# Kernel optimization log

Measured on AMD Instinct MI355X. Metric: run time of the kernel, lower is better.

The kernel has to match this reference:

```python
import jax, jax.numpy as jnp
import numpy as np

# Model constants (from init_kwargs)
NF, NC, E, B = 100000, 4000, 500000, 256
D_FACT, D_COMP = 1536, 27
HIDDEN, HEADS, CPH = 128, 4, 32  # out_per_head = hidden // heads
NUM_LAYERS = 2
TIME_DIM = 8
T_SCALE = 30.0
EDGE_DIM = 2 + TIME_DIM  # [sentiment, decay, time2vec]
ATTN_SCALE = 1.0  # 1 / attn_temperature
NEG_SLOPE = 0.2


def time_edge_features(ea, lam):
    # ea: [E, 2] = [sentiment, decay]; second column in [0,1] -> decay branch
    s = jnp.clip(ea[:, 0:1], -1.0, 1.0)
    decay = jnp.clip(ea[:, 1:2], 0.0, 1.0)
    lam = jnp.maximum(lam, 1e-6)
    delta_t = -jnp.log(jnp.maximum(decay, 1e-6)) / lam
    t = jnp.log1p(jnp.maximum(delta_t, 0.0)) / T_SCALE  # [E,1]
    freqs = jnp.arange(1, TIME_DIM, dtype=ea.dtype)      # [TIME_DIM-1]
    sins = jnp.sin(t * freqs)                            # [E,TIME_DIM-1]
    return jnp.concatenate([s, decay, sins, t], axis=-1)  # [E, EDGE_DIM]


def seg_softmax(logits, seg, n):
    # logits: [E,H]; softmax over edges sharing the same destination node
    m = jax.ops.segment_max(logits, seg, num_segments=n)
    z = jnp.exp(logits - m[seg])
    den = jax.ops.segment_sum(z, seg, num_segments=n)
    return z / (den[seg] + 1e-16)


def seg_mean(x, seg, n):
    s = jax.ops.segment_sum(x, seg, num_segments=n)
    cnt = jax.ops.segment_sum(jnp.ones((x.shape[0],), x.dtype), seg, num_segments=n)
    return s / jnp.maximum(cnt, 1.0)[:, None]


def layernorm(x, g, b, eps=1e-5):
    mu = jnp.mean(x, axis=-1, keepdims=True)
    var = jnp.var(x, axis=-1, keepdims=True)
    return (x - mu) * jax.lax.rsqrt(var + eps) * g + b


def setup_inputs() -> dict:
    key = jax.random.key(0)
    ks = jax.random.split(key, 32)

    x_fact = jax.random.normal(ks[0], (NF, D_FACT), jnp.float32)
    x_company = jax.random.normal(ks[1], (NC, D_COMP), jnp.float32)
    u = jax.random.uniform(ks[2], (E, 2), jnp.float32)
    edge_attr = jnp.concatenate([u[:, 0:1] * 2.0 - 1.0, u[:, 1:2]], axis=1)
    edge_index = jnp.stack([
        jax.random.randint(ks[3], (E,), 0, NF),
        jax.random.randint(ks[4], (E,), 0, NC),
    ]).astype(jnp.int32)
    batch_fact = jnp.sort(jax.random.randint(ks[5], (NF,), 0, B)).astype(jnp.int32)
    batch_company = jnp.sort(jax.random.randint(ks[6], (NC,), 0, B)).astype(jnp.int32)

    def p(k, shape):
        return jax.random.normal(k, shape, jnp.float32) * 0.05

    inp = dict(
        x_fact=x_fact, x_company=x_company, edge_attr=edge_attr,
        edge_index=edge_index, batch_fact=batch_fact, batch_company=batch_company,
        lambda_decay=jnp.array(0.01, jnp.float32),
        Wf=p(ks[7], (D_FACT, HIDDEN)), bf=jnp.zeros((HIDDEN,), jnp.float32),
        Wc=p(ks[8], (D_COMP, HIDDEN)), bc=jnp.zeros((HIDDEN,), jnp.float32),
        Wl=p(ks[9], (NUM_LAYERS, HIDDEN, HIDDEN)), bl=jnp.zeros((NUM_LAYERS, HIDDEN), jnp.float32),
        Wr=p(ks[10], (NUM_LAYERS, HIDDEN, HIDDEN)), br=jnp.zeros((NUM_LAYERS, HIDDEN), jnp.float32),
        We=p(ks[11], (NUM_LAYERS, EDGE_DIM, HIDDEN)), be=jnp.zeros((NUM_LAYERS, HIDDEN), jnp.float32),
        att=p(ks[12], (NUM_LAYERS, HEADS, CPH)),
        bias_out=jnp.zeros((NUM_LAYERS, HIDDEN), jnp.float32),
        ln_g=jnp.ones((NUM_LAYERS, HIDDEN), jnp.float32), ln_b=jnp.zeros((NUM_LAYERS, HIDDEN), jnp.float32),
        Wg=p(ks[13], (2 * HIDDEN, 1)), bg=jnp.zeros((1,), jnp.float32),
        W1=p(ks[14], (HIDDEN, HIDDEN)), b1=jnp.zeros((HIDDEN,), jnp.float32),
        W2=p(ks[15], (HIDDEN, 1)), b2=jnp.zeros((1,), jnp.float32),
    )
    return inp


def reference(x_fact, x_company, edge_attr, edge_index, batch_fact, batch_company,
              lambda_decay, Wf, bf, Wc, bc, Wl, bl, Wr, br, We, be, att, bias_out,
              ln_g, ln_b, Wg, bg, W1, b1, W2, b2):
    src, dst = edge_index[0], edge_index[1]
    ef = time_edge_features(edge_attr, lambda_decay)          # [E, EDGE_DIM]

    # per-node-type input encoders
    hf = jax.nn.relu(x_fact @ Wf + bf)                         # [NF, H]
    hc = jax.nn.relu(x_company @ Wc + bc)                      # [NC, H]
    n_c = x_company.shape[0]

    for l in range(NUM_LAYERS):
        # GATv2 (edge-conditioned, bipartite fact->company, share_weights=False)
        gl = (hf @ Wl[l] + bl[l]).reshape(-1, HEADS, CPH)      # src transform [NF,H,C]
        gr = (hc @ Wr[l] + br[l]).reshape(-1, HEADS, CPH)      # dst transform [NC,H,C]
        ge = (ef @ We[l] + be[l]).reshape(-1, HEADS, CPH)      # edge transform [E,H,C]
        e = jax.nn.leaky_relu(gl[src] + gr[dst] + ge, NEG_SLOPE)  # [E,H,C]
        logits = jnp.einsum('ehc,hc->eh', e, att[l]) * ATTN_SCALE  # [E,H]
        alpha = seg_softmax(logits, dst, n_c)                   # scatter-softmax over dst
        msg = alpha[..., None] * gl[src]                        # [E,H,C]
        out = jax.ops.segment_sum(msg, dst, num_segments=n_c).reshape(n_c, HIDDEN) + bias_out[l]
        hc = layernorm(hc + jax.nn.relu(out), ln_g[l], ln_b[l])  # residual + post-norm

    # gated readout over graphs in batch
    pf = seg_mean(hf, batch_fact, B)                            # [B,H]
    pc = seg_mean(hc, batch_company, B)                         # [B,H]
    g = jax.nn.sigmoid(jnp.concatenate([pf, pc], axis=-1) @ Wg + bg)  # [B,1]
    h = g * pf + (1.0 - g) * pc                                 # [B,H]
    logit = jax.nn.relu(h @ W1 + b1) @ W2 + b2                  # [B,1]
    return logit
```

## Files before the change

kernel.cpp:

```cpp
#include <hip/hip_runtime.h>
#include <hip/hip_bf16.h>
#include <math.h>

#define NFAC 100000
#define NCOMP 4000
#define NEDGE 500000
#define NB 256
#define DF 1536
#define DC 27
#define H 128
#define EDIM 10

typedef __attribute__((ext_vector_type(8))) short short8v;
typedef __attribute__((ext_vector_type(4))) float f32x4;

#define GLOAD_LDS16(g, l)                                                              \
  __builtin_amdgcn_global_load_lds((const __attribute__((address_space(1))) unsigned int*)(g), \
                                   (__attribute__((address_space(3))) unsigned int*)(l), 16, 0, 0)

__device__ __forceinline__ float group32_sum(float v) {
#pragma unroll
  for (int m = 16; m > 0; m >>= 1) v += __shfl_xor(v, m);
  return v;
}

__device__ __forceinline__ unsigned short bf16rn(float x) {
  unsigned int u = __float_as_uint(x);
  unsigned int r = (u + 0x7fffu + ((u >> 16) & 1u)) >> 16;
  return (unsigned short)r;
}
__device__ __forceinline__ float bf16tof(unsigned short h) {
  return __uint_as_float(((unsigned int)h) << 16);
}

__global__ void k_edge_feat(const float* __restrict__ ea, const float* __restrict__ lamp,
                            float* __restrict__ ef) {
  int e = blockIdx.x * blockDim.x + threadIdx.x;
  if (e >= NEDGE) return;
  float s   = fminf(fmaxf(ea[2 * e], -1.f), 1.f);
  float dec = fminf(fmaxf(ea[2 * e + 1], 0.f), 1.f);
  float lam = fmaxf(lamp[0], 1e-6f);
  float dt  = -logf(fmaxf(dec, 1e-6f)) / lam;
  float t   = log1pf(fmaxf(dt, 0.f)) * (1.f / 30.f);
  float* o = ef + (size_t)e * EDIM;
  o[0] = s;
  o[1] = dec;
#pragma unroll
  for (int k = 1; k < 8; k++) o[1 + k] = __sinf(t * (float)k);
  o[9] = t;
}

__global__ void k_hist(const int* __restrict__ dst, int* __restrict__ deg) {
  int e = blockIdx.x * blockDim.x + threadIdx.x;
  if (e < NEDGE) atomicAdd(&deg[dst[e]], 1);
}

__global__ __launch_bounds__(1024) void k_scan(const int* __restrict__ deg, int* __restrict__ off) {
  __shared__ int s[4096];
  int t = threadIdx.x;
  for (int i = t; i < 4096; i += 1024) s[i] = (i < NCOMP) ? deg[i] : 0;
  __syncthreads();
  for (int d = 1; d < 4096; d <<= 1) {
    int vals[4];
#pragma unroll
    for (int j = 0; j < 4; j++) {
      int i = t + j * 1024;
      vals[j] = (i >= d) ? s[i - d] : 0;
    }
    __syncthreads();
#pragma unroll
    for (int j = 0; j < 4; j++) {
      int i = t + j * 1024;
      s[i] += vals[j];
    }
    __syncthreads();
  }
  for (int i = t; i < 4096; i += 1024) off[i + 1] = s[i];
  if (t == 0) off[0] = 0;
}

__global__ void k_scatter(const int* __restrict__ dst, const int* __restrict__ off,
                          int* __restrict__ cur, int* __restrict__ eid) {
  int e = blockIdx.x * blockDim.x + threadIdx.x;
  if (e < NEDGE) {
    int d = dst[e];
    int p = atomicAdd(&cur[d], 1);
    eid[off[d] + p] = e;
  }
}

__global__ void k_conv_w(const float* __restrict__ W, unsigned short* __restrict__ Bh,
                         unsigned short* __restrict__ Bl, int K) {
  int i = blockIdx.x * blockDim.x + threadIdx.x;
  if (i >= K * H) return;
  int k = i >> 7, c = i & 127;
  float x = W[i];
  unsigned short h = bf16rn(x);
  unsigned short l = bf16rn(x - bf16tof(h));
  Bh[(size_t)c * K + k] = h;
  Bl[(size_t)c * K + k] = l;
}

__device__ __forceinline__ unsigned int packhi(unsigned int u1, unsigned int u0) {
  return __builtin_amdgcn_perm(u1, u0, 0x07060302u);
}

__global__ __launch_bounds__(256, 2) void k_gemm_mfma(const float* __restrict__ A,
                                                      const unsigned short* __restrict__ Bth,
                                                      const unsigned short* __restrict__ Btl,
                                                      const float* __restrict__ bias,
                                                      float* __restrict__ C, int M, int K,
                                                      int dorelu, float* __restrict__ Cpart) {
  __shared__ __align__(16) char smem[2][32768];
  int tid = threadIdx.x;
  int wave = tid >> 6, lane = tid & 63;
  int m0 = blockIdx.x * 128;
  int wm = (wave >> 1) * 64, wn = (wave & 1) * 64;
  int fr = lane & 15, fg = lane >> 4;
  int nsplit = gridDim.y;
  int Ks = K / nsplit;
  int kbeg = blockIdx.y * Ks;
  int nIter = Ks >> 5;

  f32x4 acc[4][4];
#pragma unroll
  for (int i = 0; i < 4; i++)
#pragma unroll
    for (int j = 0; j < 4; j++) acc[i][j] = (f32x4){0.f, 0.f, 0.f, 0.f};

  int a_row = (lane >> 3);
  int a_s = lane & 7;
  int b_col = (lane >> 2);
  int b_s = lane & 3;

  auto stage = [&](int buf, int k0) {
    char* base = smem[buf];
#pragma unroll
    for (int q = 0; q < 4; q++) {
      int j = wave + 4 * q;
      int row = j * 8 + a_row;
      int grow = m0 + row;
      if (grow >= M) grow = 0;
      const float* src = A + (size_t)grow * K + k0 + ((a_s ^ (row & 7)) << 2);
      GLOAD_LDS16(src, base + j * 1024);
    }
#pragma unroll
    for (int q = 0; q < 2; q++) {
      int j = wave + 4 * q;
      int col = j * 16 + b_col;
      int soff = k0 + ((b_s ^ (col & 3)) << 3);
      GLOAD_LDS16(Bth + (size_t)col * K + soff, base + 16384 + j * 1024);
      GLOAD_LDS16(Btl + (size_t)col * K + soff, base + 24576 + j * 1024);
    }
  };

  stage(0, kbeg);
  __syncthreads();

  for (int it = 0; it < nIter; ++it) {
    int cur = it & 1;
    if (it + 1 < nIter) stage(cur ^ 1, kbeg + ((it + 1) << 5));
    const char* cb = smem[cur];
    short8v ah[4], al[4];
#pragma unroll
    for (int mf = 0; mf < 4; mf++) {
      int r = wm + 16 * mf + fr;
      int s0 = (2 * fg) ^ (r & 7);
      int s1 = (2 * fg + 1) ^ (r & 7);
      float4 a0 = *(const float4*)(cb + r * 128 + s0 * 16);
      float4 a1 = *(const float4*)(cb + r * 128 + s1 * 16);
      float xs[8] = {a0.x, a0.y, a0.z, a0.w, a1.x, a1.y, a1.z, a1.w};
      unsigned int hu[8], lu[8];
#pragma unroll
      for (int j = 0; j < 8; j++) {
        unsigned int u = __float_as_uint(xs[j]);
        hu[j] = u & 0xffff0000u;
        lu[j] = __float_as_uint(xs[j] - __uint_as_float(hu[j]));
      }
      unsigned int hw[4], lw[4];
#pragma unroll
      for (int j = 0; j < 4; j++) {
        hw[j] = packhi(hu[2 * j + 1], hu[2 * j]);
        lw[j] = packhi(lu[2 * j + 1], lu[2 * j]);
      }
      ah[mf] = *(short8v*)hw;
      al[mf] = *(short8v*)lw;
    }
#pragma unroll
    for (int nf = 0; nf < 4; nf++) {
      int c = wn + 16 * nf + fr;
      int sb = fg ^ (c & 3);
      short8v bh = *(const short8v*)(cb + 16384 + c * 64 + sb * 16);
      short8v bl = *(const short8v*)(cb + 24576 + c * 64 + sb * 16);
#pragma unroll
      for (int mf = 0; mf < 4; mf++) {
        acc[mf][nf] = __builtin_amdgcn_mfma_f32_16x16x32_bf16(ah[mf], bh, acc[mf][nf], 0, 0, 0);
        acc[mf][nf] = __builtin_amdgcn_mfma_f32_16x16x32_bf16(ah[mf], bl, acc[mf][nf], 0, 0, 0);
        acc[mf][nf] = __builtin_amdgcn_mfma_f32_16x16x32_bf16(al[mf], bh, acc[mf][nf], 0, 0, 0);
      }
    }
    __syncthreads();
  }

  if (nsplit == 1) {
#pragma unroll
    for (int mf = 0; mf < 4; mf++) {
      int rbase = m0 + wm + 16 * mf + 4 * fg;
#pragma unroll
      for (int nf = 0; nf < 4; nf++) {
        int col = wn + 16 * nf + fr;
        float bv = bias[col];
#pragma unroll
        for (int j = 0; j < 4; j++) {
          int row = rbase + j;
          if (row < M) {
            float v = acc[mf][nf][j] + bv;
            if (dorelu) v = fmaxf(v, 0.f);
            C[(size_t)row * H + col] = v;
          }
        }
      }
    }
  } else {
    float* P = Cpart + (size_t)blockIdx.y * M * H;
#pragma unroll
    for (int mf = 0; mf < 4; mf++) {
      int rbase = m0 + wm + 16 * mf + 4 * fg;
#pragma unroll
      for (int nf = 0; nf < 4; nf++) {
        int col = wn + 16 * nf + fr;
#pragma unroll
        for (int j = 0; j < 4; j++) {
          int row = rbase + j;
          if (row < M) P[(size_t)row * H + col] = acc[mf][nf][j];
        }
      }
    }
  }
}

__global__ __launch_bounds__(256) void k_reduce2(const float* __restrict__ P0,
                                                 const float* __restrict__ P1,
                                                 const float* __restrict__ bias,
                                                 float* __restrict__ C, int total4) {
  int i = blockIdx.x * blockDim.x + threadIdx.x;
  if (i >= total4) return;
  float4 a = ((const float4*)P0)[i];
  float4 b = ((const float4*)P1)[i];
  float4 bv = ((const float4*)bias)[i & 31];
  float4 r;
  r.x = fmaxf(a.x + b.x + bv.x, 0.f);
  r.y = fmaxf(a.y + b.y + bv.y, 0.f);
  r.z = fmaxf(a.z + b.z + bv.z, 0.f);
  r.w = fmaxf(a.w + b.w + bv.w, 0.f);
  ((float4*)C)[i] = r;
}

__global__ void k_enc_comp(const float* __restrict__ X, const float* __restrict__ Wc,
                           const float* __restrict__ bc, float* __restrict__ hc) {
  int tid = threadIdx.x;
  int r = blockIdx.x * 2 + (tid >> 7);
  int j = tid & 127;
  if (r >= NCOMP) return;
  float acc = bc[j];
  const float* x = X + (size_t)r * DC;
#pragma unroll
  for (int k = 0; k < DC; k++) acc = fmaf(x[k], Wc[k * H + j], acc);
  hc[(size_t)r * H + j] = fmaxf(acc, 0.f);
}

__global__ __launch_bounds__(128) void k_node(
    const float* __restrict__ gl, const float* __restrict__ ef, const int* __restrict__ srcArr,
    const int* __restrict__ csr_off, const int* __restrict__ csr_eid,
    const float* __restrict__ Wr, const float* __restrict__ br, const float* __restrict__ We,
    const float* __restrict__ be, const float* __restrict__ att,
    const float* __restrict__ bias_out, const float* __restrict__ lng,
    const float* __restrict__ lnb, float* __restrict__ hc) {
  int v = blockIdx.x;
  int t = threadIdx.x;
  __shared__ float hcs[H];
  __shared__ float WeS[EDIM * H];
  __shared__ float red[2], redq[2];
  float x = hc[(size_t)v * H + t];
  hcs[t] = x;
#pragma unroll
  for (int i = 0; i < EDIM; i++) WeS[i * H + t] = We[i * H + t];
  __syncthreads();
  float grv = br[t];
  for (int k = 0; k < H; k++) grv = fmaf(hcs[k], Wr[k * H + t], grv);
  float attv = att[t];
  float bev = be[t];
  int e0 = csr_off[v], e1 = csr_off[v + 1];
  float m = -INFINITY, s = 0.f, acc = 0.f;
  for (int i = e0; i < e1; ++i) {
    int eid = csr_eid[i];
    int sid = srcArr[eid];
    float glv = gl[(size_t)sid * H + t];
    const float* efr = ef + (size_t)eid * EDIM;
    float ge = bev;
#pragma unroll
    for (int k = 0; k < EDIM; k++) ge = fmaf(efr[k], WeS[k * H + t], ge);
    float ev = glv + grv + ge;
    ev = ev > 0.f ? ev : 0.2f * ev;
    float logit = group32_sum(ev * attv);
    float mn = fmaxf(m, logit);
    float scale = __expf(m - mn);
    float z = __expf(logit - mn);
    s = s * scale + z;
    acc = acc * scale + z * glv;
    m = mn;
  }
  float outv = acc / (s + 1e-16f);
  outv += bias_out[t];
  outv = fmaxf(outv, 0.f);
  float y = x + outv;
  float sv = y, qv = y * y;
#pragma unroll
  for (int mm = 32; mm > 0; mm >>= 1) {
    sv += __shfl_xor(sv, mm);
    qv += __shfl_xor(qv, mm);
  }
  int wid = t >> 6, lane = t & 63;
  if (lane == 0) {
    red[wid] = sv;
    redq[wid] = qv;
  }
  __syncthreads();
  float mean = (red[0] + red[1]) * (1.f / H);
  float var = (redq[0] + redq[1]) * (1.f / H) - mean * mean;
  float r = rsqrtf(var + 1e-5f);
  hc[(size_t)v * H + t] = (y - mean) * r * lng[t] + lnb[t];
}

template <int CHUNK>
__global__ __launch_bounds__(128) void k_segmean(const float* __restrict__ X,
                                                 const int* __restrict__ seg, int n,
                                                 float* __restrict__ sum, int* __restrict__ cnt) {
  int t = threadIdx.x;
  int n0 = blockIdx.x * CHUNK;
  int n1 = min(n0 + CHUNK, n);
  float acc = 0.f;
  int c = 0;
  int curs = -1;
  for (int i = n0; i < n1; ++i) {
    int sg = seg[i];
    if (sg != curs) {
      if (curs >= 0) {
        atomicAdd(&sum[(size_t)curs * H + t], acc);
        if (t == 0) atomicAdd(&cnt[curs], c);
      }
      curs = sg;
      acc = 0.f;
      c = 0;
    }
    acc += X[(size_t)i * H + t];
    c++;
  }
  if (curs >= 0) {
    atomicAdd(&sum[(size_t)curs * H + t], acc);
    if (t == 0) atomicAdd(&cnt[curs], c);
  }
}

__global__ __launch_bounds__(128) void k_readout(const float* __restrict__ pf,
                                                 const float* __restrict__ pc,
                                                 const int* __restrict__ cf,
                                                 const int* __restrict__ cc,
                                                 const float* __restrict__ Wg,
                                                 const float* __restrict__ bg,
                                                 const float* __restrict__ W1,
                                                 const float* __restrict__ b1,
                                                 const float* __restrict__ W2,
                                                 const float* __restrict__ b2,
                                                 float* __restrict__ out) {
  int b = blockIdx.x, t = threadIdx.x;
  __shared__ float hs[H];
  __shared__ float red[2], red2[2];
  int wid = t >> 6, lane = t & 63;
  float nf = fmaxf((float)cf[b], 1.f);
  float nc = fmaxf((float)cc[b], 1.f);
  float pfv = pf[(size_t)b * H + t] / nf;
  float pcv = pc[(size_t)b * H + t] / nc;
  float gp = pfv * Wg[t] + pcv * Wg[H + t];
  float sv = gp;
#pragma unroll
  for (int mm = 32; mm > 0; mm >>= 1) sv += __shfl_xor(sv, mm);
  if (lane == 0) red[wid] = sv;
  __syncthreads();
  float g = 1.f / (1.f + expf(-(red[0] + red[1] + bg[0])));
  float h = g * pfv + (1.f - g) * pcv;
  hs[t] = h;
  __syncthreads();
  float a = b1[t];
  for (int k = 0; k < H; k++) a = fmaf(hs[k], W1[k * H + t], a);
  a = fmaxf(a, 0.f);
  float p = a * W2[t];
#pragma unroll
  for (int mm = 32; mm > 0; mm >>= 1) p += __shfl_xor(p, mm);
  if (lane == 0) red2[wid] = p;
  __syncthreads();
  if (t == 0) out[b] = red2[0] + red2[1] + b2[0];
}

extern "C" void kernel_launch(void* const* d_in, const int* in_sizes, int n_in, void* d_out,
                              int out_size, void* d_ws, size_t ws_size, hipStream_t stream) {
  const float* x_fact = (const float*)d_in[0];
  const float* x_comp = (const float*)d_in[1];
  const float* ea = (const float*)d_in[2];
  const int* eidx = (const int*)d_in[3];
  const int* batf = (const int*)d_in[4];
  const int* batc = (const int*)d_in[5];
  const float* lam = (const float*)d_in[6];
  const float* Wf = (const float*)d_in[7];
  const float* bf = (const float*)d_in[8];
  const float* Wc = (const float*)d_in[9];
  const float* bc = (const float*)d_in[10];
  const float* Wl = (const float*)d_in[11];
  const float* bl = (const float*)d_in[12];
  const float* Wr = (const float*)d_in[13];
  const float* br_ = (const float*)d_in[14];
  const float* We = (const float*)d_in[15];
  const float* be = (const float*)d_in[16];
  const float* att = (const float*)d_in[17];
  const float* b_out = (const float*)d_in[18];
  const float* lng = (const float*)d_in[19];
  const float* lnb = (const float*)d_in[20];
  const float* Wg = (const float*)d_in[21];
  const float* bg = (const float*)d_in[22];
  const float* W1 = (const float*)d_in[23];
  const float* b1 = (const float*)d_in[24];
  const float* W2 = (const float*)d_in[25];
  const float* b2 = (const float*)d_in[26];
  float* out = (float*)d_out;

  char* w = (char*)d_ws;
  auto carve = [&](size_t bytes) -> char* {
    char* p = w;
    w += (bytes + 255) & ~(size_t)255;
    return p;
  };
  float* HF = (float*)carve((size_t)NFAC * H * 4);
  float* GL = (float*)carve((size_t)NFAC * H * 4);
  float* CP1 = (float*)carve((size_t)NFAC * H * 4);
  float* HC = (float*)carve((size_t)NCOMP * H * 4);
  float* EF = (float*)carve((size_t)NEDGE * EDIM * 4);
  int* OFF = (int*)carve(4100 * 4);
  int* EID = (int*)carve((size_t)NEDGE * 4);
  unsigned short* WfH = (unsigned short*)carve((size_t)DF * H * 2);
  unsigned short* WfL = (unsigned short*)carve((size_t)DF * H * 2);
  unsigned short* WlH[2], *WlL[2];
  for (int l = 0; l < 2; l++) {
    WlH[l] = (unsigned short*)carve((size_t)H * H * 2);
    WlL[l] = (unsigned short*)carve((size_t)H * H * 2);
  }
  char* zbase = w;
  int* DEG = (int*)carve(4096 * 4);
  int* CUR = (int*)carve(4096 * 4);
  float* PF = (float*)carve((size_t)NB * H * 4);
  float* PC = (float*)carve((size_t)NB * H * 4);
  int* CF = (int*)carve(NB * 4);
  int* CC = (int*)carve(NB * 4);
  size_t zbytes = (size_t)(w - zbase);
  hipMemsetAsync(zbase, 0, zbytes, stream);

  const int* srcArr = eidx;
  const int* dstArr = eidx + NEDGE;

  k_edge_feat<<<(NEDGE + 255) / 256, 256, 0, stream>>>(ea, lam, EF);
  k_hist<<<(NEDGE + 255) / 256, 256, 0, stream>>>(dstArr, DEG);
  k_scan<<<1, 1024, 0, stream>>>(DEG, OFF);
  k_scatter<<<(NEDGE + 255) / 256, 256, 0, stream>>>(dstArr, OFF, CUR, EID);

  k_conv_w<<<(DF * H + 255) / 256, 256, 0, stream>>>(Wf, WfH, WfL, DF);
  for (int l = 0; l < 2; l++)
    k_conv_w<<<(H * H + 255) / 256, 256, 0, stream>>>(Wl + (size_t)l * H * H, WlH[l], WlL[l], H);

  {
    float* CPART = GL;
    dim3 grid((NFAC + 127) / 128, 2);
    k_gemm_mfma<<<grid, 256, 0, stream>>>(x_fact, WfH, WfL, bf, HF, NFAC, DF, 1, CPART);
    int total4 = NFAC * H / 4;
    k_reduce2<<<(total4 + 255) / 256, 256, 0, stream>>>(GL, CP1, bf, HF, total4);
  }
  k_enc_comp<<<NCOMP / 2, 256, 0, stream>>>(x_comp, Wc, bc, HC);

  for (int l = 0; l < 2; l++) {
    dim3 grid((NFAC + 127) / 128, 1);
    k_gemm_mfma<<<grid, 256, 0, stream>>>(HF, WlH[l], WlL[l], bl + l * H, GL, NFAC, H, 0,
                                          (float*)nullptr);
    k_node<<<NCOMP, 128, 0, stream>>>(GL, EF, srcArr, OFF, EID, Wr + (size_t)l * H * H,
                                      br_ + l * H, We + (size_t)l * EDIM * H, be + l * H,
                                      att + l * H, b_out + l * H, lng + l * H, lnb + l * H, HC);
  }

  k_segmean<128><<<(NFAC + 127) / 128, 128, 0, stream>>>(HF, batf, NFAC, PF, CF);
  k_segmean<64><<<(NCOMP + 63) / 64, 128, 0, stream>>>(HC, batc, NCOMP, PC, CC);
  k_readout<<<NB, 128, 0, stream>>>(PF, PC, CF, CC, Wg, bg, W1, b1, W2, b2, out);
}
```

Measured before the change: 765.3 us.

## Split per-node edge loop across four thread groups with online-softmax merge

The node attention kernel now runs 512 threads per company node, with four 128-thread groups each handling every fourth incoming edge. Each group keeps its own running max, sum and accumulator, and these are merged through shared memory with a log-sum-exp combine before the residual and layernorm. The next edge's index and source id are also prefetched inside the loop to hide the dependent load latency. This shortens the serial chain of about 125 edges per node and adds parallelism. The cost is that each group recomputes the 128x128 Wr projection, and there is extra shared memory and a block barrier.

Result: slower. 844.1 us (+10.3%).

```diff
diff --git a/kernel.cpp b/kernel.cpp
--- a/kernel.cpp
+++ b/kernel.cpp
@@ -269,7 +269,8 @@
   hc[(size_t)r * H + j] = fmaxf(acc, 0.f);
 }
 
-__global__ __launch_bounds__(128) void k_node(
+#define NG 4
+__global__ __launch_bounds__(512) void k_node(
     const float* __restrict__ gl, const float* __restrict__ ef, const int* __restrict__ srcArr,
     const int* __restrict__ csr_off, const int* __restrict__ csr_eid,
     const float* __restrict__ Wr, const float* __restrict__ br, const float* __restrict__ We,
@@ -277,29 +278,44 @@
     const float* __restrict__ bias_out, const float* __restrict__ lng,
     const float* __restrict__ lnb, float* __restrict__ hc) {
   int v = blockIdx.x;
-  int t = threadIdx.x;
+  int tid = threadIdx.x;
+  int g = tid >> 7;
+  int t = tid & 127;
   __shared__ float hcs[H];
   __shared__ float WeS[EDIM * H];
+  __shared__ float gmA[NG][H];
+  __shared__ float gsA[NG][H];
+  __shared__ float gaA[NG][H];
   __shared__ float red[2], redq[2];
-  float x = hc[(size_t)v * H + t];
-  hcs[t] = x;
-#pragma unroll
-  for (int i = 0; i < EDIM; i++) WeS[i * H + t] = We[i * H + t];
-  __syncthreads();
+  if (tid < H) hcs[tid] = hc[(size_t)v * H + tid];
+  for (int i = tid; i < EDIM * H; i += 512) WeS[i] = We[i];
+  __syncthreads();
+
   float grv = br[t];
   for (int k = 0; k < H; k++) grv = fmaf(hcs[k], Wr[k * H + t], grv);
   float attv = att[t];
   float bev = be[t];
+
   int e0 = csr_off[v], e1 = csr_off[v + 1];
   float m = -INFINITY, s = 0.f, acc = 0.f;
-  for (int i = e0; i < e1; ++i) {
-    int eid = csr_eid[i];
-    int sid = srcArr[eid];
+  int i = e0 + g;
+  int eid = 0, sid = 0;
+  if (i < e1) {
+    eid = csr_eid[i];
+    sid = srcArr[eid];
+  }
+  while (i < e1) {
     float glv = gl[(size_t)sid * H + t];
     const float* efr = ef + (size_t)eid * EDIM;
     float ge = bev;
 #pragma unroll
     for (int k = 0; k < EDIM; k++) ge = fmaf(efr[k], WeS[k * H + t], ge);
+    int ni = i + NG;
+    if (ni < e1) {
+      int ne = csr_eid[ni];
+      eid = ne;
+      sid = srcArr[ne];
+    }
     float ev = glv + grv + ge;
     ev = ev > 0.f ? ev : 0.2f * ev;
     float logit = group32_sum(ev * attv);
@@ -309,27 +325,48 @@
     s = s * scale + z;
     acc = acc * scale + z * glv;
     m = mn;
-  }
-  float outv = acc / (s + 1e-16f);
-  outv += bias_out[t];
-  outv = fmaxf(outv, 0.f);
-  float y = x + outv;
-  float sv = y, qv = y * y;
-#pragma unroll
-  for (int mm = 32; mm > 0; mm >>= 1) {
-    sv += __shfl_xor(sv, mm);
-    qv += __shfl_xor(qv, mm);
-  }
-  int wid = t >> 6, lane = t & 63;
-  if (lane == 0) {
-    red[wid] = sv;
-    redq[wid] = qv;
-  }
-  __syncthreads();
-  float mean = (red[0] + red[1]) * (1.f / H);
-  float var = (redq[0] + redq[1]) * (1.f / H) - mean * mean;
-  float r = rsqrtf(var + 1e-5f);
-  hc[(size_t)v * H + t] = (y - mean) * r * lng[t] + lnb[t];
+    i = ni;
+  }
+  gmA[g][t] = m;
+  gsA[g][t] = s;
+  gaA[g][t] = acc;
+  __syncthreads();
+
+  float y = 0.f;
+  if (tid < H) {
+    float mstar = gmA[0][t];
+#pragma unroll
+    for (int q = 1; q < NG; q++) mstar = fmaxf(mstar, gmA[q][t]);
+    float sstar = 0.f, astar = 0.f;
+#pragma unroll
+    for (int q = 0; q < NG; q++) {
+      float mg = gmA[q][t];
+      float w = (mg > -INFINITY) ? __expf(mg - mstar) : 0.f;
+      sstar += gsA[q][t] * w;
+      astar += gaA[q][t] * w;
+    }
+    float outv = astar / (sstar + 1e-16f);
+    outv += bias_out[t];
+    outv = fmaxf(outv, 0.f);
+    y = hcs[t] + outv;
+    float sv = y, qv = y * y;
+#pragma unroll
+    for (int mm = 32; mm > 0; mm >>= 1) {
+      sv += __shfl_xor(sv, mm);
+      qv += __shfl_xor(qv, mm);
+    }
+    if ((t & 63) == 0) {
+      red[t >> 6] = sv;
+      redq[t >> 6] = qv;
+    }
+  }
+  __syncthreads();
+  if (tid < H) {
+    float mean = (red[0] + red[1]) * (1.f / H);
+    float var = (redq[0] + redq[1]) * (1.f / H) - mean * mean;
+    float r = rsqrtf(var + 1e-5f);
+    hc[(size_t)v * H + t] = (y - mean) * r * lng[t] + lnb[t];
+  }
 }
 
 template <int CHUNK>
@@ -488,7 +525,7 @@
     dim3 grid((NFAC + 127) / 128, 1);
     k_gemm_mfma<<<grid, 256, 0, stream>>>(HF, WlH[l], WlL[l], bl + l * H, GL, NFAC, H, 0,
                                           (float*)nullptr);
-    k_node<<<NCOMP, 128, 0, stream>>>(GL, EF, srcArr, OFF, EID, Wr + (size_t)l * H * H,
+    k_node<<<NCOMP, 512, 0, stream>>>(GL, EF, srcArr, OFF, EID, Wr + (size_t)l * H * H,
                                       br_ + l * H, We + (size_t)l * EDIM * H, be + l * H,
                                       att + l * H, b_out + l * H, lng + l * H, lnb + l * H, HC);
   }
```
